# Performance work log

Measured on AMD Instinct MI355X. Metric: run time of the kernel, lower is better.

Reference implementation:

```python
import jax, jax.numpy as jnp
import numpy as np

D = 2            # stalk dimension d
FD = 3           # final_d = d + 1 (add_lp=True, add_hp=False)
HID = 32         # hidden_channels
N_NODES = 50000
E0 = 200000      # undirected edges; directed edge list has 2*E0 entries (second half reversed)
IN_CH = 128
OUT_CH = 32
N_LAYERS = 2
PSIZE = D * (D + 1) // 2  # cayley param size per edge


def _spectral_normalize(W, iters=20):
    # torch spectral_norm: power iteration with detached u, v; sigma = u^T W v
    u = jnp.full((W.shape[0],), 1.0 / np.sqrt(W.shape[0]), W.dtype)
    def body(_, u):
        v = W.T @ u
        v = v / (jnp.linalg.norm(v) + 1e-12)
        u2 = W @ v
        return u2 / (jnp.linalg.norm(u2) + 1e-12)
    u = jax.lax.fori_loop(0, iters, body, u)
    u = jax.lax.stop_gradient(u)
    v = jax.lax.stop_gradient(W.T @ u)
    v = v / (jnp.linalg.norm(v) + 1e-12)
    return W / (u @ W @ v)


def _cayley(p):
    # p: [E, PSIZE] lower-tri params -> skew A -> orthogonal Q = (I - A)^{-1}(I + A)
    E = p.shape[0]
    r, c = jnp.tril_indices(D)
    M = jnp.zeros((E, D, D), p.dtype).at[:, r, c].set(p)
    A = M - jnp.swapaxes(M, 1, 2)
    I = jnp.eye(D, dtype=p.dtype)
    return jnp.linalg.solve(I[None] - A, I[None] + A)


def setup_inputs() -> dict:
    key = jax.random.key(0)
    ks = jax.random.split(key, 8)
    src = jax.random.randint(ks[0], (E0,), 0, N_NODES)
    dst = jax.random.randint(ks[1], (E0,), 0, N_NODES)
    # symmetric directed edge list; edge j and edge j+E0 are reverses of each other
    edge_index = jnp.concatenate([jnp.stack([src, dst]), jnp.stack([dst, src])], axis=1)
    x = jax.random.normal(ks[2], (N_NODES, IN_CH), jnp.float32)
    s = 0.02
    W1 = jax.random.normal(ks[3], (FD * HID, IN_CH), jnp.float32) * s
    b1 = jnp.zeros((FD * HID,), jnp.float32)
    W2 = jax.random.normal(ks[4], (OUT_CH, FD * HID), jnp.float32) * s
    b2 = jnp.zeros((OUT_CH,), jnp.float32)
    W_left = jnp.tile(jnp.eye(FD, dtype=jnp.float32)[None], (N_LAYERS, 1, 1))  # init eye per torch
    W_right = jax.random.normal(ks[5], (N_LAYERS, HID, HID), jnp.float32) / np.sqrt(HID)
    eps = jnp.zeros((N_LAYERS, FD, 1), jnp.float32)
    W_sheaf = jax.random.normal(ks[6], (N_LAYERS, PSIZE, 2 * FD * HID), jnp.float32) * s
    W_wt = jax.random.normal(ks[7], (N_LAYERS, 1, 2 * FD * HID), jnp.float32) * s
    return {"x": x, "edge_index": edge_index, "W1": W1, "b1": b1, "W2": W2, "b2": b2,
            "W_left": W_left, "W_right": W_right, "eps": eps, "W_sheaf": W_sheaf, "W_wt": W_wt}


def reference(x, edge_index, W1, b1, W2, b2, W_left, W_right, eps, W_sheaf, W_wt):
    N = x.shape[0]
    row, col = edge_index[0], edge_index[1]
    e0 = row.shape[0] // 2
    rev = jnp.concatenate([jnp.arange(e0) + e0, jnp.arange(e0)])  # reverse-edge index
    # lin1 + ELU (dropouts = 0 in eval)
    h = jax.nn.elu(x @ W1.T + b1)                 # [N, FD*HID]
    xc = h.reshape(N * FD, HID)                   # [N*FD, HID]
    x0 = xc
    for layer in range(N_LAYERS):
        # --- sheaf learner + edge weight learner (gather endpoint features) ---
        xn = xc.reshape(N, FD * HID)
        cat = jnp.concatenate([xn[row], xn[col]], axis=-1)   # [2*E0, 2*FD*HID]
        p = jnp.tanh(cat @ W_sheaf[layer].T)                 # sheaf map params [2*E0, PSIZE]
        wdir = jax.nn.sigmoid(cat @ W_wt[layer].T)[:, 0]
        w = wdir * wdir[rev]                                 # symmetric edge weight
        # --- normalized connection (bundle) Laplacian ---
        Q = _cayley(p)                                       # per-edge orthogonal maps
        T = jnp.einsum('eij,eik->ejk', Q, Q[rev])            # transport F_u^T F_v
        w2 = w * w
        deg = jax.ops.segment_sum(w2, row, num_segments=N)
        dinv = jnp.where(deg > 0, jax.lax.rsqrt(jnp.maximum(deg, 1e-30)), 0.0)
        cnorm = w2 * dinv[row] * dinv[col]                   # [2*E0]
        # --- left / right weights (spectral-normalized) ---
        Wl = _spectral_normalize(W_left[layer])
        Wr = _spectral_normalize(W_right[layer])
        y = xc.reshape(N, FD, HID)
        y = jnp.einsum('ef,nfh->neh', Wl, y)                 # mix stalk dims
        y = jnp.einsum('neh,ch->nec', y, Wr)                 # mix channels
        # --- apply block-sparse Laplacian: Lx[u] = x[u] - sum_e c_e B_e x[v] ---
        yv = y[col]                                          # gather  [2*E0, FD, HID]
        tv = jnp.concatenate([jnp.einsum('eij,ejh->eih', T, yv[:, :D]), yv[:, D:]], axis=1)
        agg = jax.ops.segment_sum(cnorm[:, None, None] * tv, row, num_segments=N)
        diag = jnp.where(deg > 0, 1.0, 0.0)[:, None, None]
        z = jax.nn.elu((diag * y - agg).reshape(N * FD, HID))
        # --- epsilon-gated residual ---
        coeff = jnp.tile(1.0 + jnp.tanh(eps[layer]), (N, 1))  # [N*FD, 1]
        x0 = coeff * x0 - z
        xc = x0
    return xc.reshape(N, FD * HID) @ W2.T + b2
```

## Files before the change

### kernel.cpp

```cpp
#include <hip/hip_runtime.h>
#include <hip/hip_bf16.h>

#define NN   50000
#define E0   200000
#define E2   400000

typedef __attribute__((ext_vector_type(8))) short short8;
typedef __attribute__((ext_vector_type(4))) float f32x4;

__device__ __forceinline__ float eluf(float x) { return x > 0.0f ? x : expm1f(x); }
__device__ __forceinline__ float sigmoidf(float x) { return 1.0f / (1.0f + expf(-x)); }
__device__ __forceinline__ unsigned rne_bf16(float x) {
    unsigned u = __float_as_uint(x);
    return (u + 0x7fffu + ((u >> 16) & 1u)) >> 16;
}

__global__ __launch_bounds__(256) void k_splitw(const float* __restrict__ W, int n,
                                                unsigned short* __restrict__ hi,
                                                unsigned short* __restrict__ lo) {
    int i = blockIdx.x * 256 + threadIdx.x;
    if (i >= n) return;
    float x = W[i];
    unsigned h = rne_bf16(x);
    hi[i] = (unsigned short)h;
    lo[i] = (unsigned short)rne_bf16(x - __uint_as_float(h << 16));
}

template<int K, int N, bool ELU>
__global__ __launch_bounds__(256) void k_gemm_mfma(const float* __restrict__ X,
                                                   const unsigned short* __restrict__ Whi,
                                                   const unsigned short* __restrict__ Wlo,
                                                   const float* __restrict__ bias,
                                                   float* __restrict__ out) {
    constexpr int KP = K + 8;
    constexpr int NT = N / 16;
    constexpr int KS = K / 32;
    __shared__ __align__(16) unsigned short whi[N * KP];
    __shared__ __align__(16) unsigned short wlo[N * KP];
    int tid = threadIdx.x;
    for (int i = tid; i < N * K / 2; i += 256) {
        unsigned vh = ((const unsigned*)Whi)[i];
        unsigned vl = ((const unsigned*)Wlo)[i];
        int e = i * 2, r = e / K, c = e % K;
        *(unsigned*)&whi[r * KP + c] = vh;
        *(unsigned*)&wlo[r * KP + c] = vl;
    }
    __syncthreads();
    int wave = tid >> 6, lane = tid & 63;
    int quad = lane >> 4, r16 = lane & 15;
    long m = (long)blockIdx.x * 64 + wave * 16 + r16;
    long mc = m < NN ? m : (NN - 1);
    const float* xrow = X + mc * K + quad * 8;
    f32x4 acc[NT];
#pragma unroll
    for (int t = 0; t < NT; ++t) acc[t] = (f32x4){0.f, 0.f, 0.f, 0.f};
#pragma unroll
    for (int ks = 0; ks < KS; ++ks) {
        const float4* xp = (const float4*)(xrow + ks * 32);
        float4 p0 = xp[0], p1 = xp[1];
        float xv[8] = {p0.x, p0.y, p0.z, p0.w, p1.x, p1.y, p1.z, p1.w};
        short8 a_hi, a_lo;
#pragma unroll
        for (int j = 0; j < 8; ++j) {
            unsigned h = rne_bf16(xv[j]);
            a_hi[j] = (short)h;
            a_lo[j] = (short)rne_bf16(xv[j] - __uint_as_float(h << 16));
        }
#pragma unroll
        for (int t = 0; t < NT; ++t) {
            int ro = (t * 16 + r16) * KP + ks * 32 + quad * 8;
            short8 bh = *(const short8*)&whi[ro];
            short8 bl = *(const short8*)&wlo[ro];
            acc[t] = __builtin_amdgcn_mfma_f32_16x16x32_bf16(a_hi, bh, acc[t], 0, 0, 0);
            acc[t] = __builtin_amdgcn_mfma_f32_16x16x32_bf16(a_lo, bh, acc[t], 0, 0, 0);
            acc[t] = __builtin_amdgcn_mfma_f32_16x16x32_bf16(a_hi, bl, acc[t], 0, 0, 0);
        }
    }
    long mbase = (long)blockIdx.x * 64 + wave * 16 + quad * 4;
#pragma unroll
    for (int t = 0; t < NT; ++t) {
        float b = bias[t * 16 + r16];
#pragma unroll
        for (int rr = 0; rr < 4; ++rr) {
            long mm = mbase + rr;
            if (mm < NN) {
                float v = acc[t][rr] + b;
                if (ELU) v = eluf(v);
                out[mm * N + t * 16 + r16] = v;
            }
        }
    }
}

__global__ __launch_bounds__(64) void k_spectral(const float* __restrict__ Wl_in,
                                                 const float* __restrict__ Wr_in,
                                                 float* __restrict__ Wl_out,
                                                 float* __restrict__ Wr_out) {
    int l = blockIdx.x, t = threadIdx.x;
    __shared__ float W[32 * 33];
    __shared__ float us[32], vs[32], tmp[32];
    __shared__ float scal;
    for (int i = t; i < 1024; i += 64) W[(i >> 5) * 33 + (i & 31)] = Wr_in[l * 1024 + i];
    if (t < 32) us[t] = 0.17677669529663688f;
    __syncthreads();
    for (int it = 0; it < 20; ++it) {
        if (t < 32) { float a = 0; for (int r = 0; r < 32; ++r) a = fmaf(W[r * 33 + t], us[r], a); tmp[t] = a; }
        __syncthreads();
        if (t == 0) { float s = 0; for (int c = 0; c < 32; ++c) s += tmp[c] * tmp[c]; scal = 1.0f / (sqrtf(s) + 1e-12f); }
        __syncthreads();
        if (t < 32) vs[t] = tmp[t] * scal;
        __syncthreads();
        if (t < 32) { float a = 0; for (int c = 0; c < 32; ++c) a = fmaf(W[t * 33 + c], vs[c], a); tmp[t] = a; }
        __syncthreads();
        if (t == 0) { float s = 0; for (int r = 0; r < 32; ++r) s += tmp[r] * tmp[r]; scal = 1.0f / (sqrtf(s) + 1e-12f); }
        __syncthreads();
        if (t < 32) us[t] = tmp[t] * scal;
        __syncthreads();
    }
    if (t < 32) { float a = 0; for (int r = 0; r < 32; ++r) a = fmaf(W[r * 33 + t], us[r], a); tmp[t] = a; }
    __syncthreads();
    if (t == 0) {
        float s = 0; for (int c = 0; c < 32; ++c) s += tmp[c] * tmp[c];
        scal = (sqrtf(s) + 1e-12f) / s;
    }
    __syncthreads();
    for (int i = t; i < 1024; i += 64) Wr_out[l * 1024 + i] = W[(i >> 5) * 33 + (i & 31)] * scal;

    if (t == 0) {
        float M[9];
        for (int i = 0; i < 9; ++i) M[i] = Wl_in[l * 9 + i];
        float u[3] = {0.5773502691896258f, 0.5773502691896258f, 0.5773502691896258f};
        float v[3], u2[3];
        for (int it = 0; it < 20; ++it) {
            float s = 0;
            for (int c = 0; c < 3; ++c) { v[c] = M[c] * u[0] + M[3 + c] * u[1] + M[6 + c] * u[2]; s += v[c] * v[c]; }
            float inv = 1.0f / (sqrtf(s) + 1e-12f);
            for (int c = 0; c < 3; ++c) v[c] *= inv;
            s = 0;
            for (int r = 0; r < 3; ++r) { u2[r] = M[r * 3] * v[0] + M[r * 3 + 1] * v[1] + M[r * 3 + 2] * v[2]; s += u2[r] * u2[r]; }
            inv = 1.0f / (sqrtf(s) + 1e-12f);
            for (int r = 0; r < 3; ++r) u[r] = u2[r] * inv;
        }
        float s = 0;
        for (int c = 0; c < 3; ++c) { v[c] = M[c] * u[0] + M[3 + c] * u[1] + M[6 + c] * u[2]; s += v[c] * v[c]; }
        float inv = (sqrtf(s) + 1e-12f) / s;
        for (int i = 0; i < 9; ++i) Wl_out[l * 9 + i] = M[i] * inv;
    }
}

__global__ __launch_bounds__(256) void k_hist(const int* __restrict__ row, int* __restrict__ cnt) {
    int e = blockIdx.x * 256 + threadIdx.x;
    if (e < E2) atomicAdd(&cnt[row[e]], 1);
}
__global__ __launch_bounds__(256) void k_scan1(const int* __restrict__ cnt, int* __restrict__ start,
                                               int* __restrict__ bsum) {
    __shared__ int s[256];
    int b = blockIdx.x, t = threadIdx.x;
    int i = b * 256 + t;
    int v = (i < NN) ? cnt[i] : 0;
    s[t] = v;
    __syncthreads();
    for (int off = 1; off < 256; off <<= 1) {
        int add = (t >= off) ? s[t - off] : 0;
        __syncthreads();
        s[t] += add;
        __syncthreads();
    }
    if (i < NN) start[i] = s[t] - v;
    if (t == 255) bsum[b] = s[t];
}
__global__ __launch_bounds__(256) void k_scan2(const int* __restrict__ bsum, int* __restrict__ bofs,
                                               int nb) {
    __shared__ int s[256];
    int t = threadIdx.x;
    int v = (t < nb) ? bsum[t] : 0;
    s[t] = v;
    __syncthreads();
    for (int off = 1; off < 256; off <<= 1) {
        int add = (t >= off) ? s[t - off] : 0;
        __syncthreads();
        s[t] += add;
        __syncthreads();
    }
    if (t < nb) bofs[t] = s[t] - v;
}
__global__ __launch_bounds__(256) void k_scan3(int* __restrict__ start, const int* __restrict__ bofs) {
    int i = blockIdx.x * 256 + threadIdx.x;
    if (i < NN) start[i] += bofs[i >> 8];
}
__global__ __launch_bounds__(256) void k_fill(const int* __restrict__ row, const int* __restrict__ start,
                                              int* __restrict__ fill, int* __restrict__ eslot) {
    int e = blockIdx.x * 256 + threadIdx.x;
    if (e >= E2) return;
    int u = row[e];
    eslot[e] = start[u] + atomicAdd(&fill[u], 1);
}

__global__ __launch_bounds__(256) void k_y8(const float* __restrict__ xc,
                                            const float* __restrict__ Wl,
                                            const float* __restrict__ Wr,
                                            const float* __restrict__ Wsh,
                                            const float* __restrict__ Wwt,
                                            int layer,
                                            unsigned* __restrict__ yp01,
                                            unsigned short* __restrict__ yp2,
                                            float* __restrict__ aR, float* __restrict__ aC,
                                            float* __restrict__ wR, float* __restrict__ wC,
                                            float* __restrict__ deg) {
    __shared__ float wrs[32 * 33];
    __shared__ float wls[9];
    __shared__ float xcs[8][96];
    __shared__ float ws1[192], wt[192];
    int tid = threadIdx.x;
    int n0 = blockIdx.x * 8;
    if (tid < 8) { int nz = n0 + tid; if (nz < NN) deg[nz] = 0.0f; }
    for (int i = tid; i < 1024; i += 256) wrs[(i >> 5) * 33 + (i & 31)] = Wr[i];
    if (tid < 9) wls[tid] = Wl[tid];
    if (tid < 192) {
        ws1[tid] = Wsh[(layer * 3 + 1) * 192 + tid];
        wt[tid]  = Wwt[layer * 192 + tid];
    }
    for (int i = tid; i < 768; i += 256) {
        int n = n0 + i / 96;
        xcs[i / 96][i % 96] = (n < NN) ? xc[n * 96 + i % 96] : 0.0f;
    }
    __syncthreads();
    int node = tid >> 5, c = tid & 31;
    int n = n0 + node;
    float a1 = 0, a2 = 0, a3 = 0, a4 = 0;
#pragma unroll
    for (int j = 0; j < 3; ++j) {
        int k = j * 32 + c;
        float xv = xcs[node][k];
        a1 = fmaf(xv, ws1[k], a1);
        a2 = fmaf(xv, ws1[96 + k], a2);
        a3 = fmaf(xv, wt[k], a3);
        a4 = fmaf(xv, wt[96 + k], a4);
    }
#pragma unroll
    for (int off = 16; off; off >>= 1) {
        a1 += __shfl_xor(a1, off);
        a2 += __shfl_xor(a2, off);
        a3 += __shfl_xor(a3, off);
        a4 += __shfl_xor(a4, off);
    }
    if (c == 0 && n < NN) { aR[n] = a1; aC[n] = a2; wR[n] = a3; wC[n] = a4; }
    if (n < NN) {
        float t0 = 0, t1 = 0, t2 = 0;
        const float* wr = &wrs[c * 33];
        const float* xr = xcs[node];
#pragma unroll
        for (int h = 0; h < 32; ++h) {
            float w = wr[h];
            t0 = fmaf(xr[h], w, t0);
            t1 = fmaf(xr[32 + h], w, t1);
            t2 = fmaf(xr[64 + h], w, t2);
        }
        float o0 = wls[0] * t0 + wls[1] * t1 + wls[2] * t2;
        float o1 = wls[3] * t0 + wls[4] * t1 + wls[5] * t2;
        float o2 = wls[6] * t0 + wls[7] * t1 + wls[8] * t2;
        yp01[n * 32 + c] = rne_bf16(o0) | (rne_bf16(o1) << 16);
        yp2[n * 32 + c]  = (unsigned short)rne_bf16(o2);
    }
}

__global__ __launch_bounds__(256) void k_edge_coef(const int* __restrict__ row, const int* __restrict__ col,
                                                   const int* __restrict__ eslot,
                                                   const float* __restrict__ aR, const float* __restrict__ aC,
                                                   const float* __restrict__ wR, const float* __restrict__ wC,
                                                   float4* __restrict__ meta, float* __restrict__ deg) {
    int e = blockIdx.x * 256 + threadIdx.x;
    if (e >= E0) return;
    int u = row[e], v = col[e];
    float a_e = tanhf(aR[u] + aC[v]);
    float a_r = tanhf(aR[v] + aC[u]);
    float wd_e = sigmoidf(wR[u] + wC[v]);
    float wd_r = sigmoidf(wR[v] + wC[u]);
    float w = wd_e * wd_r;
    float w2 = w * w;
    float ie = 1.0f / (1.0f + a_e * a_e), ir = 1.0f / (1.0f + a_r * a_r);
    float ce = (1.0f - a_e * a_e) * ie, se = 2.0f * a_e * ie;
    float cr = (1.0f - a_r * a_r) * ir, sr = 2.0f * a_r * ir;
    float C = ce * cr + se * sr;
    float S = ce * sr - se * cr;
    meta[eslot[e]]      = make_float4(C,  S, w2, __int_as_float(v));
    meta[eslot[e + E0]] = make_float4(C, -S, w2, __int_as_float(u));
    atomicAdd(&deg[u], w2);
    atomicAdd(&deg[v], w2);
}

__global__ __launch_bounds__(256) void k_dinv(const float* __restrict__ deg, float* __restrict__ dinv) {
    int n = blockIdx.x * 256 + threadIdx.x;
    if (n >= NN) return;
    float d = deg[n];
    dinv[n] = d > 0.0f ? rsqrtf(fmaxf(d, 1e-30f)) : 0.0f;
}

__global__ __launch_bounds__(256) void k_gather_update(const int* __restrict__ start, const int* __restrict__ cnt,
                                                       const float4* __restrict__ meta,
                                                       const float* __restrict__ dinv,
                                                       const unsigned* __restrict__ yp01,
                                                       const unsigned short* __restrict__ yp2,
                                                       const float* __restrict__ eps,
                                                       int layer, float* __restrict__ xc) {
    int tid = threadIdx.x;
    int node = tid >> 5, c = tid & 31;
    int n = blockIdx.x * 8 + node;
    if (n >= NN) return;
    int s0 = start[n], ec = cnt[n];
    float du = dinv[n];
    float acc0 = 0, acc1 = 0, acc2 = 0;
    for (int bs = 0; bs < ec; bs += 32) {
        int nb = min(32, ec - bs);
        float CC = 0, SS = 0, cnl = 0;
        int vj = 0;
        if (c < nb) {
            float4 mt = meta[s0 + bs + c];
            vj = __float_as_int(mt.w);
            cnl = mt.z * du * dinv[vj];
            CC = cnl * mt.x;
            SS = cnl * mt.y;
        }
        for (int j = 0; j < nb; ++j) {
            float Cj = __shfl(CC, j, 32);
            float Sj = __shfl(SS, j, 32);
            float cj = __shfl(cnl, j, 32);
            int v = __shfl(vj, j, 32);
            unsigned u01 = yp01[v * 32 + c];
            unsigned u2v = (unsigned)yp2[v * 32 + c];
            float y0 = __uint_as_float(u01 << 16);
            float y1 = __uint_as_float(u01 & 0xffff0000u);
            float y2 = __uint_as_float(u2v << 16);
            acc0 = fmaf(Cj, y0, acc0);
            acc0 = fmaf(-Sj, y1, acc0);
            acc1 = fmaf(Sj, y0, acc1);
            acc1 = fmaf(Cj, y1, acc1);
            acc2 = fmaf(cj, y2, acc2);
        }
    }
    float diag = du > 0.0f ? 1.0f : 0.0f;
    unsigned u01 = yp01[n * 32 + c];
    unsigned u2v = (unsigned)yp2[n * 32 + c];
    float oy0 = __uint_as_float(u01 << 16);
    float oy1 = __uint_as_float(u01 & 0xffff0000u);
    float oy2 = __uint_as_float(u2v << 16);
    float c0 = 1.0f + tanhf(eps[layer * 3 + 0]);
    float c1 = 1.0f + tanhf(eps[layer * 3 + 1]);
    float c2 = 1.0f + tanhf(eps[layer * 3 + 2]);
    int base = n * 96 + c;
    float z0 = eluf(diag * oy0 - acc0);
    float z1 = eluf(diag * oy1 - acc1);
    float z2 = eluf(diag * oy2 - acc2);
    xc[base]      = c0 * xc[base]      - z0;
    xc[base + 32] = c1 * xc[base + 32] - z1;
    xc[base + 64] = c2 * xc[base + 64] - z2;
}

extern "C" void kernel_launch(void* const* d_in, const int* in_sizes, int n_in,
                              void* d_out, int out_size, void* d_ws, size_t ws_size,
                              hipStream_t stream) {
    const float* x     = (const float*)d_in[0];
    const int*   ei    = (const int*)d_in[1];
    const float* W1    = (const float*)d_in[2];
    const float* b1    = (const float*)d_in[3];
    const float* W2    = (const float*)d_in[4];
    const float* bias2 = (const float*)d_in[5];
    const float* Wl_in = (const float*)d_in[6];
    const float* Wr_in = (const float*)d_in[7];
    const float* eps   = (const float*)d_in[8];
    const float* Wsh   = (const float*)d_in[9];
    const float* Wwt   = (const float*)d_in[10];
    float* out = (float*)d_out;
    const int* row = ei;
    const int* col = ei + E2;

    char* pc = (char*)d_ws;
    float* xc    = (float*)pc;          pc += (size_t)NN * 96 * 4;
    float4* meta = (float4*)pc;         pc += (size_t)E2 * 16;
    unsigned* yp01 = (unsigned*)pc;     pc += (size_t)NN * 32 * 4;
    unsigned short* yp2 = (unsigned short*)pc; pc += (size_t)NN * 32 * 2;
    float* aR    = (float*)pc;          pc += (size_t)NN * 4;
    float* aC    = (float*)pc;          pc += (size_t)NN * 4;
    float* wRp   = (float*)pc;          pc += (size_t)NN * 4;
    float* wCp   = (float*)pc;          pc += (size_t)NN * 4;
    float* deg   = (float*)pc;          pc += (size_t)NN * 4;
    float* dinv  = (float*)pc;          pc += (size_t)NN * 4;
    float* Wl_n  = (float*)pc;          pc += 32 * 4;
    float* Wr_n  = (float*)pc;          pc += 2048 * 4;
    int* cnt     = (int*)pc;            pc += (size_t)NN * 4;
    int* start   = (int*)pc;            pc += (size_t)NN * 4;
    int* fill    = (int*)pc;            pc += (size_t)NN * 4;
    int* eslot   = (int*)pc;            pc += (size_t)E2 * 4;
    int* bsum    = (int*)pc;            pc += 256 * 4;
    int* bofs    = (int*)pc;            pc += 256 * 4;
    unsigned short* w1hi = (unsigned short*)pc; pc += 96 * 128 * 2;
    unsigned short* w1lo = (unsigned short*)pc; pc += 96 * 128 * 2;
    unsigned short* w2hi = (unsigned short*)pc; pc += 32 * 96 * 2;
    unsigned short* w2lo = (unsigned short*)pc; pc += 32 * 96 * 2;

    const int NB  = (NN + 255) / 256;
    const int EB  = (E2 + 255) / 256;
    const int EB0 = (E0 + 255) / 256;
    const int MB  = (NN + 63) / 64;

    k_splitw<<<(96 * 128 + 255) / 256, 256, 0, stream>>>(W1, 96 * 128, w1hi, w1lo);
    k_splitw<<<(32 * 96 + 255) / 256, 256, 0, stream>>>(W2, 32 * 96, w2hi, w2lo);
    k_gemm_mfma<128, 96, true><<<MB, 256, 0, stream>>>(x, w1hi, w1lo, b1, xc);
    k_spectral<<<2, 64, 0, stream>>>(Wl_in, Wr_in, Wl_n, Wr_n);

    hipMemsetAsync(cnt, 0, NN * sizeof(int), stream);
    hipMemsetAsync(fill, 0, NN * sizeof(int), stream);
    k_hist<<<EB, 256, 0, stream>>>(row, cnt);
    k_scan1<<<NB, 256, 0, stream>>>(cnt, start, bsum);
    k_scan2<<<1, 256, 0, stream>>>(bsum, bofs, NB);
    k_scan3<<<NB, 256, 0, stream>>>(start, bofs);
    k_fill<<<EB, 256, 0, stream>>>(row, start, fill, eslot);

    for (int l = 0; l < 2; ++l) {
        k_y8<<<(NN + 7) / 8, 256, 0, stream>>>(xc, Wl_n + l * 9, Wr_n + l * 1024, Wsh, Wwt, l,
                                               yp01, yp2, aR, aC, wRp, wCp, deg);
        k_edge_coef<<<EB0, 256, 0, stream>>>(row, col, eslot, aR, aC, wRp, wCp, meta, deg);
        k_dinv<<<NB, 256, 0, stream>>>(deg, dinv);
        k_gather_update<<<(NN + 7) / 8, 256, 0, stream>>>(start, cnt, meta, dinv,
                                                          yp01, yp2, eps, l, xc);
    }
    k_gemm_mfma<96, 32, false><<<MB, 256, 0, stream>>>(xc, w2hi, w2lo, bias2, out);
}
```

Baseline: 377.6 us.

## Merge setup kernels, fuse histogram into GEMM, drop scan3, pack y into uint2

The weight bf16 splitting, spectral normalization and buffer zeroing move into one setup kernel, replacing two memsets and three launches. The edge-degree histogram is folded into the tail of the first GEMM kernel. The third scan pass is dropped by adding the block offset at each use site. The two separate bf16 y buffers become one uint2 array, so each neighbour gather is a single 8-byte load, at the cost of two unused padding bytes per element. The main aim is fewer launches and one fewer memory access per gathered neighbour.

```diff
diff --git a/kernel.cpp b/kernel.cpp
--- a/kernel.cpp
+++ b/kernel.cpp
@@ -1,9 +1,11 @@
 #include <hip/hip_runtime.h>
-#include <hip/hip_bf16.h>
-
-#define NN   50000
-#define E0   200000
-#define E2   400000
+
+#define NN 50000
+#define E0 200000
+#define E2 400000
+#define NGROUPS ((NN + 7) / 8)
+#define NCHUNK  ((NN + 255) / 256)
+#define NTILES  ((NN + 63) / 64)
 
 typedef __attribute__((ext_vector_type(8))) short short8;
 typedef __attribute__((ext_vector_type(4))) float f32x4;
@@ -15,23 +17,90 @@
     return (u + 0x7fffu + ((u >> 16) & 1u)) >> 16;
 }
 
-__global__ __launch_bounds__(256) void k_splitw(const float* __restrict__ W, int n,
-                                                unsigned short* __restrict__ hi,
-                                                unsigned short* __restrict__ lo) {
-    int i = blockIdx.x * 256 + threadIdx.x;
-    if (i >= n) return;
-    float x = W[i];
-    unsigned h = rne_bf16(x);
-    hi[i] = (unsigned short)h;
-    lo[i] = (unsigned short)rne_bf16(x - __uint_as_float(h << 16));
-}
-
-template<int K, int N, bool ELU>
-__global__ __launch_bounds__(256) void k_gemm_mfma(const float* __restrict__ X,
-                                                   const unsigned short* __restrict__ Whi,
-                                                   const unsigned short* __restrict__ Wlo,
-                                                   const float* __restrict__ bias,
-                                                   float* __restrict__ out) {
+__global__ __launch_bounds__(256) void k_setup(const float* __restrict__ W1, const float* __restrict__ W2,
+                                               const float* __restrict__ Wl_in, const float* __restrict__ Wr_in,
+                                               float* __restrict__ Wl_out, float* __restrict__ Wr_out,
+                                               unsigned short* __restrict__ w1hi, unsigned short* __restrict__ w1lo,
+                                               unsigned short* __restrict__ w2hi, unsigned short* __restrict__ w2lo,
+                                               int* __restrict__ cnt, int* __restrict__ fill,
+                                               float* __restrict__ deg) {
+    __shared__ float W[32 * 33];
+    __shared__ float us[32], vs[32], tmp[32];
+    __shared__ float scal;
+    int t = threadIdx.x;
+    if (blockIdx.x < 2) {
+        int l = blockIdx.x;
+        for (int i = t; i < 1024; i += 256) W[(i >> 5) * 33 + (i & 31)] = Wr_in[l * 1024 + i];
+        if (t < 32) us[t] = 0.17677669529663688f;
+        __syncthreads();
+        for (int it = 0; it < 20; ++it) {
+            if (t < 32) { float a = 0; for (int r = 0; r < 32; ++r) a = fmaf(W[r * 33 + t], us[r], a); tmp[t] = a; }
+            __syncthreads();
+            if (t == 0) { float s = 0; for (int c = 0; c < 32; ++c) s += tmp[c] * tmp[c]; scal = 1.0f / (sqrtf(s) + 1e-12f); }
+            __syncthreads();
+            if (t < 32) vs[t] = tmp[t] * scal;
+            __syncthreads();
+            if (t < 32) { float a = 0; for (int c = 0; c < 32; ++c) a = fmaf(W[t * 33 + c], vs[c], a); tmp[t] = a; }
+            __syncthreads();
+            if (t == 0) { float s = 0; for (int r = 0; r < 32; ++r) s += tmp[r] * tmp[r]; scal = 1.0f / (sqrtf(s) + 1e-12f); }
+            __syncthreads();
+            if (t < 32) us[t] = tmp[t] * scal;
+            __syncthreads();
+        }
+        if (t < 32) { float a = 0; for (int r = 0; r < 32; ++r) a = fmaf(W[r * 33 + t], us[r], a); tmp[t] = a; }
+        __syncthreads();
+        if (t == 0) {
+            float s = 0; for (int c = 0; c < 32; ++c) s += tmp[c] * tmp[c];
+            scal = (sqrtf(s) + 1e-12f) / s;
+        }
+        __syncthreads();
+        for (int i = t; i < 1024; i += 256) Wr_out[l * 1024 + i] = W[(i >> 5) * 33 + (i & 31)] * scal;
+        if (t == 0) {
+            float M[9];
+            for (int i = 0; i < 9; ++i) M[i] = Wl_in[l * 9 + i];
+            float u[3] = {0.5773502691896258f, 0.5773502691896258f, 0.5773502691896258f};
+            float v[3], u2[3];
+            for (int it = 0; it < 20; ++it) {
+                float s = 0;
+                for (int c = 0; c < 3; ++c) { v[c] = M[c] * u[0] + M[3 + c] * u[1] + M[6 + c] * u[2]; s += v[c] * v[c]; }
+                float inv = 1.0f / (sqrtf(s) + 1e-12f);
+                for (int c = 0; c < 3; ++c) v[c] *= inv;
+                s = 0;
+                for (int r = 0; r < 3; ++r) { u2[r] = M[r * 3] * v[0] + M[r * 3 + 1] * v[1] + M[r * 3 + 2] * v[2]; s += u2[r] * u2[r]; }
+                inv = 1.0f / (sqrtf(s) + 1e-12f);
+                for (int r = 0; r < 3; ++r) u[r] = u2[r] * inv;
+            }
+            float s = 0;
+            for (int c = 0; c < 3; ++c) { v[c] = M[c] * u[0] + M[3 + c] * u[1] + M[6 + c] * u[2]; s += v[c] * v[c]; }
+            float inv = (sqrtf(s) + 1e-12f) / s;
+            for (int i = 0; i < 9; ++i) Wl_out[l * 9 + i] = M[i] * inv;
+        }
+    } else {
+        int base = (blockIdx.x - 2) * 256 + t;
+        int stride = (gridDim.x - 2) * 256;
+        for (int i = base; i < 96 * 128; i += stride) {
+            float v = W1[i];
+            unsigned h = rne_bf16(v);
+            w1hi[i] = (unsigned short)h;
+            w1lo[i] = (unsigned short)rne_bf16(v - __uint_as_float(h << 16));
+        }
+        for (int i = base; i < 32 * 96; i += stride) {
+            float v = W2[i];
+            unsigned h = rne_bf16(v);
+            w2hi[i] = (unsigned short)h;
+            w2lo[i] = (unsigned short)rne_bf16(v - __uint_as_float(h << 16));
+        }
+        for (int i = base; i < NN; i += stride) { cnt[i] = 0; fill[i] = 0; deg[i] = 0.0f; }
+    }
+}
+
+template<int K, int N, bool ELU, bool HIST>
+__global__ __launch_bounds__(256) void k_gemm(const float* __restrict__ X,
+                                              const unsigned short* __restrict__ Whi,
+                                              const unsigned short* __restrict__ Wlo,
+                                              const float* __restrict__ bias,
+                                              float* __restrict__ out,
+                                              const int* __restrict__ row, int* __restrict__ cnt) {
     constexpr int KP = K + 8;
     constexpr int NT = N / 16;
     constexpr int KS = K / 32;
@@ -90,68 +159,12 @@
             }
         }
     }
-}
-
-__global__ __launch_bounds__(64) void k_spectral(const float* __restrict__ Wl_in,
-                                                 const float* __restrict__ Wr_in,
-                                                 float* __restrict__ Wl_out,
-                                                 float* __restrict__ Wr_out) {
-    int l = blockIdx.x, t = threadIdx.x;
-    __shared__ float W[32 * 33];
-    __shared__ float us[32], vs[32], tmp[32];
-    __shared__ float scal;
-    for (int i = t; i < 1024; i += 64) W[(i >> 5) * 33 + (i & 31)] = Wr_in[l * 1024 + i];
-    if (t < 32) us[t] = 0.17677669529663688f;
-    __syncthreads();
-    for (int it = 0; it < 20; ++it) {
-        if (t < 32) { float a = 0; for (int r = 0; r < 32; ++r) a = fmaf(W[r * 33 + t], us[r], a); tmp[t] = a; }
-        __syncthreads();
-        if (t == 0) { float s = 0; for (int c = 0; c < 32; ++c) s += tmp[c] * tmp[c]; scal = 1.0f / (sqrtf(s) + 1e-12f); }
-        __syncthreads();
-        if (t < 32) vs[t] = tmp[t] * scal;
-        __syncthreads();
-        if (t < 32) { float a = 0; for (int c = 0; c < 32; ++c) a = fmaf(W[t * 33 + c], vs[c], a); tmp[t] = a; }
-        __syncthreads();
-        if (t == 0) { float s = 0; for (int r = 0; r < 32; ++r) s += tmp[r] * tmp[r]; scal = 1.0f / (sqrtf(s) + 1e-12f); }
-        __syncthreads();
-        if (t < 32) us[t] = tmp[t] * scal;
-        __syncthreads();
-    }
-    if (t < 32) { float a = 0; for (int r = 0; r < 32; ++r) a = fmaf(W[r * 33 + t], us[r], a); tmp[t] = a; }
-    __syncthreads();
-    if (t == 0) {
-        float s = 0; for (int c = 0; c < 32; ++c) s += tmp[c] * tmp[c];
-        scal = (sqrtf(s) + 1e-12f) / s;
-    }
-    __syncthreads();
-    for (int i = t; i < 1024; i += 64) Wr_out[l * 1024 + i] = W[(i >> 5) * 33 + (i & 31)] * scal;
-
-    if (t == 0) {
-        float M[9];
-        for (int i = 0; i < 9; ++i) M[i] = Wl_in[l * 9 + i];
-        float u[3] = {0.5773502691896258f, 0.5773502691896258f, 0.5773502691896258f};
-        float v[3], u2[3];
-        for (int it = 0; it < 20; ++it) {
-            float s = 0;
-            for (int c = 0; c < 3; ++c) { v[c] = M[c] * u[0] + M[3 + c] * u[1] + M[6 + c] * u[2]; s += v[c] * v[c]; }
-            float inv = 1.0f / (sqrtf(s) + 1e-12f);
-            for (int c = 0; c < 3; ++c) v[c] *= inv;
-            s = 0;
-            for (int r = 0; r < 3; ++r) { u2[r] = M[r * 3] * v[0] + M[r * 3 + 1] * v[1] + M[r * 3 + 2] * v[2]; s += u2[r] * u2[r]; }
-            inv = 1.0f / (sqrtf(s) + 1e-12f);
-            for (int r = 0; r < 3; ++r) u[r] = u2[r] * inv;
-        }
-        float s = 0;
-        for (int c = 0; c < 3; ++c) { v[c] = M[c] * u[0] + M[3 + c] * u[1] + M[6 + c] * u[2]; s += v[c] * v[c]; }
-        float inv = (sqrtf(s) + 1e-12f) / s;
-        for (int i = 0; i < 9; ++i) Wl_out[l * 9 + i] = M[i] * inv;
-    }
-}
-
-__global__ __launch_bounds__(256) void k_hist(const int* __restrict__ row, int* __restrict__ cnt) {
-    int e = blockIdx.x * 256 + threadIdx.x;
-    if (e < E2) atomicAdd(&cnt[row[e]], 1);
-}
+    if (HIST) {
+        for (int e = blockIdx.x * 256 + tid; e < E2; e += gridDim.x * 256)
+            atomicAdd(&cnt[row[e]], 1);
+    }
+}
+
 __global__ __launch_bounds__(256) void k_scan1(const int* __restrict__ cnt, int* __restrict__ start,
                                                int* __restrict__ bsum) {
     __shared__ int s[256];
@@ -169,8 +182,7 @@
     if (i < NN) start[i] = s[t] - v;
     if (t == 255) bsum[b] = s[t];
 }
-__global__ __launch_bounds__(256) void k_scan2(const int* __restrict__ bsum, int* __restrict__ bofs,
-                                               int nb) {
+__global__ __launch_bounds__(256) void k_scan2(const int* __restrict__ bsum, int* __restrict__ bofs, int nb) {
     __shared__ int s[256];
     int t = threadIdx.x;
     int v = (t < nb) ? bsum[t] : 0;
@@ -184,26 +196,19 @@
     }
     if (t < nb) bofs[t] = s[t] - v;
 }
-__global__ __launch_bounds__(256) void k_scan3(int* __restrict__ start, const int* __restrict__ bofs) {
-    int i = blockIdx.x * 256 + threadIdx.x;
-    if (i < NN) start[i] += bofs[i >> 8];
-}
 __global__ __launch_bounds__(256) void k_fill(const int* __restrict__ row, const int* __restrict__ start,
+                                              const int* __restrict__ bofs,
                                               int* __restrict__ fill, int* __restrict__ eslot) {
     int e = blockIdx.x * 256 + threadIdx.x;
     if (e >= E2) return;
     int u = row[e];
-    eslot[e] = start[u] + atomicAdd(&fill[u], 1);
+    eslot[e] = start[u] + bofs[u >> 8] + atomicAdd(&fill[u], 1);
 }
 
 __global__ __launch_bounds__(256) void k_y8(const float* __restrict__ xc,
-                                            const float* __restrict__ Wl,
-                                            const float* __restrict__ Wr,
-                                            const float* __restrict__ Wsh,
-                                            const float* __restrict__ Wwt,
-                                            int layer,
-                                            unsigned* __restrict__ yp01,
-                                            unsigned short* __restrict__ yp2,
+                                            const float* __restrict__ Wl, const float* __restrict__ Wr,
+                                            const float* __restrict__ Wsh, const float* __restrict__ Wwt,
+                                            int layer, uint2* __restrict__ yp,
                                             float* __restrict__ aR, float* __restrict__ aC,
                                             float* __restrict__ wR, float* __restrict__ wC,
                                             float* __restrict__ deg) {
@@ -259,16 +264,15 @@
         float o0 = wls[0] * t0 + wls[1] * t1 + wls[2] * t2;
         float o1 = wls[3] * t0 + wls[4] * t1 + wls[5] * t2;
         float o2 = wls[6] * t0 + wls[7] * t1 + wls[8] * t2;
-        yp01[n * 32 + c] = rne_bf16(o0) | (rne_bf16(o1) << 16);
-        yp2[n * 32 + c]  = (unsigned short)rne_bf16(o2);
-    }
-}
-
-__global__ __launch_bounds__(256) void k_edge_coef(const int* __restrict__ row, const int* __restrict__ col,
-                                                   const int* __restrict__ eslot,
-                                                   const float* __restrict__ aR, const float* __restrict__ aC,
-                                                   const float* __restrict__ wR, const float* __restrict__ wC,
-                                                   float4* __restrict__ meta, float* __restrict__ deg) {
+        yp[n * 32 + c] = make_uint2(rne_bf16(o0) | (rne_bf16(o1) << 16), rne_bf16(o2));
+    }
+}
+
+__global__ __launch_bounds__(256) void k_coef(const int* __restrict__ row, const int* __restrict__ col,
+                                              const int* __restrict__ eslot,
+                                              const float* __restrict__ aR, const float* __restrict__ aC,
+                                              const float* __restrict__ wR, const float* __restrict__ wC,
+                                              float4* __restrict__ meta, float* __restrict__ deg) {
     int e = blockIdx.x * 256 + threadIdx.x;
     if (e >= E0) return;
     int u = row[e], v = col[e];
@@ -296,41 +300,40 @@
     dinv[n] = d > 0.0f ? rsqrtf(fmaxf(d, 1e-30f)) : 0.0f;
 }
 
-__global__ __launch_bounds__(256) void k_gather_update(const int* __restrict__ start, const int* __restrict__ cnt,
-                                                       const float4* __restrict__ meta,
-                                                       const float* __restrict__ dinv,
-                                                       const unsigned* __restrict__ yp01,
-                                                       const unsigned short* __restrict__ yp2,
-                                                       const float* __restrict__ eps,
-                                                       int layer, float* __restrict__ xc) {
+__global__ __launch_bounds__(256) void k_gather(const int* __restrict__ start, const int* __restrict__ bofs,
+                                                const int* __restrict__ cnt,
+                                                const float4* __restrict__ meta,
+                                                const float* __restrict__ dinv,
+                                                const uint2* __restrict__ yp,
+                                                const float* __restrict__ eps,
+                                                int layer, float* __restrict__ xc) {
     int tid = threadIdx.x;
     int node = tid >> 5, c = tid & 31;
     int n = blockIdx.x * 8 + node;
     if (n >= NN) return;
-    int s0 = start[n], ec = cnt[n];
+    int s0 = start[n] + bofs[n >> 8], ec = cnt[n];
     float du = dinv[n];
     float acc0 = 0, acc1 = 0, acc2 = 0;
     for (int bs = 0; bs < ec; bs += 32) {
-        int nb = min(32, ec - bs);
+        int nb2 = min(32, ec - bs);
         float CC = 0, SS = 0, cnl = 0;
         int vj = 0;
-        if (c < nb) {
+        if (c < nb2) {
             float4 mt = meta[s0 + bs + c];
             vj = __float_as_int(mt.w);
             cnl = mt.z * du * dinv[vj];
             CC = cnl * mt.x;
             SS = cnl * mt.y;
         }
-        for (int j = 0; j < nb; ++j) {
+        for (int j = 0; j < nb2; ++j) {
             float Cj = __shfl(CC, j, 32);
             float Sj = __shfl(SS, j, 32);
             float cj = __shfl(cnl, j, 32);
             int v = __shfl(vj, j, 32);
-            unsigned u01 = yp01[v * 32 + c];
-            unsigned u2v = (unsigned)yp2[v * 32 + c];
-            float y0 = __uint_as_float(u01 << 16);
-            float y1 = __uint_as_float(u01 & 0xffff0000u);
-            float y2 = __uint_as_float(u2v << 16);
+            uint2 uy = yp[v * 32 + c];
+            float y0 = __uint_as_float(uy.x << 16);
+            float y1 = __uint_as_float(uy.x & 0xffff0000u);
+            float y2 = __uint_as_float(uy.y << 16);
             acc0 = fmaf(Cj, y0, acc0);
             acc0 = fmaf(-Sj, y1, acc0);
             acc1 = fmaf(Sj, y0, acc1);
@@ -339,11 +342,10 @@
         }
     }
     float diag = du > 0.0f ? 1.0f : 0.0f;
-    unsigned u01 = yp01[n * 32 + c];
-    unsigned u2v = (unsigned)yp2[n * 32 + c];
-    float oy0 = __uint_as_float(u01 << 16);
-    float oy1 = __uint_as_float(u01 & 0xffff0000u);
-    float oy2 = __uint_as_float(u2v << 16);
+    uint2 uy = yp[n * 32 + c];
+    float oy0 = __uint_as_float(uy.x << 16);
+    float oy1 = __uint_as_float(uy.x & 0xffff0000u);
+    float oy2 = __uint_as_float(uy.y << 16);
     float c0 = 1.0f + tanhf(eps[layer * 3 + 0]);
     float c1 = 1.0f + tanhf(eps[layer * 3 + 1]);
     float c2 = 1.0f + tanhf(eps[layer * 3 + 2]);
@@ -364,9 +366,9 @@
     const float* W1    = (const float*)d_in[2];
     const float* b1    = (const float*)d_in[3];
     const float* W2    = (const float*)d_in[4];
-    const float* bias2 = (const float*)d_in[5];
-    const float* Wl_in = (const float*)d_in[6];
-    const float* Wr_in = (const float*)d_in[7];
+    const float* b2    = (const float*)d_in[5];
+    const float* Wl    = (const float*)d_in[6];
+    const float* Wr    = (const float*)d_in[7];
     const float* eps   = (const float*)d_in[8];
     const float* Wsh   = (const float*)d_in[9];
     const float* Wwt   = (const float*)d_in[10];
@@ -377,8 +379,7 @@
     char* pc = (char*)d_ws;
     float* xc    = (float*)pc;          pc += (size_t)NN * 96 * 4;
     float4* meta = (float4*)pc;         pc += (size_t)E2 * 16;
-    unsigned* yp01 = (unsigned*)pc;     pc += (size_t)NN * 32 * 4;
-    unsigned short* yp2 = (unsigned short*)pc; pc += (size_t)NN * 32 * 2;
+    uint2* yp    = (uint2*)pc;          pc += (size_t)NN * 32 * 8;
     float* aR    = (float*)pc;          pc += (size_t)NN * 4;
     float* aC    = (float*)pc;          pc += (size_t)NN * 4;
     float* wRp   = (float*)pc;          pc += (size_t)NN * 4;
@@ -398,31 +399,20 @@
     unsigned short* w2hi = (unsigned short*)pc; pc += 32 * 96 * 2;
     unsigned short* w2lo = (unsigned short*)pc; pc += 32 * 96 * 2;
 
-    const int NB  = (NN + 255) / 256;
-    const int EB  = (E2 + 255) / 256;
-    const int EB0 = (E0 + 255) / 256;
-    const int MB  = (NN + 63) / 64;
-
-    k_splitw<<<(96 * 128 + 255) / 256, 256, 0, stream>>>(W1, 96 * 128, w1hi, w1lo);
-    k_splitw<<<(32 * 96 + 255) / 256, 256, 0, stream>>>(W2, 32 * 96, w2hi, w2lo);
-    k_gemm_mfma<128, 96, true><<<MB, 256, 0, stream>>>(x, w1hi, w1lo, b1, xc);
-    k_spectral<<<2, 64, 0, stream>>>(Wl_in, Wr_in, Wl_n, Wr_n);
-
-    hipMemsetAsync(cnt, 0, NN * sizeof(int), stream);
-    hipMemsetAsync(fill, 0, NN * sizeof(int), stream);
-    k_hist<<<EB, 256, 0, stream>>>(row, cnt);
-    k_scan1<<<NB, 256, 0, stream>>>(cnt, start, bsum);
-    k_scan2<<<1, 256, 0, stream>>>(bsum, bofs, NB);
-    k_scan3<<<NB, 256, 0, stream>>>(start, bofs);
-    k_fill<<<EB, 256, 0, stream>>>(row, start, fill, eslot);
-
+    const int EB = (E2 + 255) / 256;
+
+    k_setup<<<66, 256, 0, stream>>>(W1, W2, Wl, Wr, Wl_n, Wr_n,
+                                    w1hi, w1lo, w2hi, w2lo, cnt, fill, deg);
+    k_gemm<128, 96, true, true><<<NTILES, 256, 0, stream>>>(x, w1hi, w1lo, b1, xc, row, cnt);
+    k_scan1<<<NCHUNK, 256, 0, stream>>>(cnt, start, bsum);
+    k_scan2<<<1, 256, 0, stream>>>(bsum, bofs, NCHUNK);
+    k_fill<<<EB, 256, 0, stream>>>(row, start, bofs, fill, eslot);
     for (int l = 0; l < 2; ++l) {
-        k_y8<<<(NN + 7) / 8, 256, 0, stream>>>(xc, Wl_n + l * 9, Wr_n + l * 1024, Wsh, Wwt, l,
-                                               yp01, yp2, aR, aC, wRp, wCp, deg);
-        k_edge_coef<<<EB0, 256, 0, stream>>>(row, col, eslot, aR, aC, wRp, wCp, meta, deg);
-        k_dinv<<<NB, 256, 0, stream>>>(deg, dinv);
-        k_gather_update<<<(NN + 7) / 8, 256, 0, stream>>>(start, cnt, meta, dinv,
-                                                          yp01, yp2, eps, l, xc);
-    }
-    k_gemm_mfma<96, 32, false><<<MB, 256, 0, stream>>>(xc, w2hi, w2lo, bias2, out);
-}
+        k_y8<<<NGROUPS, 256, 0, stream>>>(xc, Wl_n + l * 9, Wr_n + l * 1024, Wsh, Wwt, l,
+                                          yp, aR, aC, wRp, wCp, deg);
+        k_coef<<<(E0 + 255) / 256, 256, 0, stream>>>(row, col, eslot, aR, aC, wRp, wCp, meta, deg);
+        k_dinv<<<NCHUNK, 256, 0, stream>>>(deg, dinv);
+        k_gather<<<NGROUPS, 256, 0, stream>>>(start, bofs, cnt, meta, dinv, yp, eps, l, xc);
+    }
+    k_gemm<96, 32, false, false><<<NTILES, 256, 0, stream>>>(xc, w2hi, w2lo, b2, out, nullptr, nullptr);
+}
```

After: 357.1 us. 5.4% less time.
